# Optimization experiments

Measured on AMD Instinct MI355X. Metric: run time of the kernel, lower is better.

## Reference

```python
import jax, jax.numpy as jnp
import numpy as np

L, H, C = 2, 2, 128            # conv layers, heads, out_channels
N, E, B = 10000, 100000, 64    # nodes, edges, graphs
F_NODE, F_EDGE, FC = 92, 50, 512
HC, C3 = H * C, 3 * C


def _ln(x, g, b, eps=1e-5):
    m = x.mean(-1, keepdims=True)
    v = jnp.var(x, axis=-1, keepdims=True)
    return (x - m) * jax.lax.rsqrt(v + eps) * g + b


def setup_inputs() -> dict:
    key = jax.random.key(0)
    ks = jax.random.split(key, 20)
    r = lambda i, shape, s=0.05: jax.random.normal(ks[i], shape, jnp.float32) * s
    d = {}
    d["x"] = jax.random.normal(ks[0], (N, F_NODE), jnp.float32)
    d["edge_attr"] = jax.random.normal(ks[1], (E, F_EDGE), jnp.float32)
    d["pge"] = jax.random.normal(ks[2], (B, 32), jnp.float32)
    d["cse"] = jax.random.normal(ks[3], (B, 7), jnp.float32)
    d["edge_index"] = jax.random.randint(ks[4], (2, E), 0, N, jnp.int32)
    d["batch"] = jnp.sort(jax.random.randint(ks[5], (N,), 0, B, jnp.int32))
    d["atom_W"] = r(6, (F_NODE, C)); d["atom_b"] = jnp.zeros(C)
    d["edge_W"] = r(7, (F_EDGE, C)); d["edge_b"] = jnp.zeros(C)
    d["Wq"] = r(8, (L, C, HC)); d["bq"] = jnp.zeros((L, HC))
    d["Wk"] = r(9, (L, C, HC)); d["bk"] = jnp.zeros((L, HC))
    d["Wv"] = r(10, (L, C, HC)); d["bv"] = jnp.zeros((L, HC))
    d["We"] = r(11, (L, C, HC))
    d["Wmu"] = r(12, (L, C3, C3)); d["bmu"] = jnp.zeros((L, C3))
    d["Wm"] = r(13, (L, C3, C)); d["bm"] = jnp.zeros((L, C))
    d["ln_m_g"] = jnp.ones((L, C)); d["ln_m_b"] = jnp.zeros((L, C))
    d["ln_a_g"] = jnp.ones((L, C3)); d["ln_a_b"] = jnp.zeros((L, C3))
    d["Wc"] = r(14, (L, HC, C)); d["bc"] = jnp.zeros((L, C))
    d["bn_g"] = jnp.ones((L, C)); d["bn_b"] = jnp.zeros((L, C))
    d["Wskip"] = r(15, (L, C, C)); d["bskip"] = jnp.zeros((L, C))
    d["fc_W"] = r(16, (C + 32 + 7, FC)); d["fc_b"] = jnp.zeros(FC)
    d["out_W"] = r(17, (FC, 1)); d["out_b"] = jnp.zeros(1)
    return d


def reference(x, edge_attr, pge, cse, edge_index, batch, atom_W, atom_b,
              edge_W, edge_b, Wq, bq, Wk, bk, Wv, bv, We, Wmu, bmu, Wm, bm,
              ln_m_g, ln_m_b, ln_a_g, ln_a_b, Wc, bc, bn_g, bn_b, Wskip,
              bskip, fc_W, fc_b, out_W, out_b):
    src, dst = edge_index[0], edge_index[1]  # j = source, i = target
    nf = x @ atom_W + atom_b                 # [N, C]
    ef = edge_attr @ edge_W + edge_b         # [E, C]
    scale = 1.0 / np.sqrt(C3).astype(np.float32)
    for i in range(L):
        q = (nf @ Wq[i] + bq[i]).reshape(N, H, C)
        k = (nf @ Wk[i] + bk[i]).reshape(N, H, C)
        v = (nf @ Wv[i] + bv[i]).reshape(N, H, C)
        ea = (ef @ We[i]).reshape(E, H, C)
        qi = q[dst]
        qcat = jnp.concatenate([qi, qi, qi], -1)                 # [E,H,3C]
        kcat = jnp.concatenate([k[dst], k[src], ea], -1)         # [E,H,3C]
        alpha = qcat * kcat * scale
        gate = jax.nn.sigmoid(_ln(alpha, ln_a_g[i], ln_a_b[i]))
        m = jnp.concatenate([v[dst], v[src], ea], -1)            # [E,H,3C]
        m = (jnp.einsum('ehf,fg->ehg', m, Wmu[i]) + bmu[i]) * gate
        m = jnp.einsum('ehf,fc->ehc', m, Wm[i]) + bm[i]          # [E,H,C]
        m = _ln(m, ln_m_g[i], ln_m_b[i])
        agg = jax.ops.segment_sum(m, dst, num_segments=N)        # scatter-add
        o = agg.reshape(N, HC) @ Wc[i] + bc[i]                   # lin_concate
        mu = o.mean(0); var = jnp.var(o, axis=0)                 # BN (batch stats)
        o = (o - mu) * jax.lax.rsqrt(var + 1e-5) * bn_g[i] + bn_b[i]
        o = jax.nn.silu(o)
        nf = o + nf @ Wskip[i] + bskip[i]                        # root skip
    sums = jax.ops.segment_sum(nf, batch, num_segments=B)
    cnt = jax.ops.segment_sum(jnp.ones((N, 1), nf.dtype), batch, num_segments=B)
    pooled = sums / jnp.maximum(cnt, 1.0)                        # global_mean_pool
    feats = jnp.concatenate([pooled, pge, cse], 1)               # [B, C+39]
    h = jax.nn.silu(feats @ fc_W + fc_b)
    return h @ out_W + out_b                                     # [B, 1]
```

## Files before the change

### kernel.cpp

```cpp
#include <hip/hip_runtime.h>
#include <math.h>

#define N_NODES 10000
#define N_EDGES 100000
#define N_GRAPH 64
#define CDIM 128
#define HCDIM 256
#define C3DIM 384
#define QKPW 2176

typedef unsigned short u16;
typedef __attribute__((ext_vector_type(8))) short bf16x8;
typedef __attribute__((ext_vector_type(4))) float f32x4;

__device__ __forceinline__ u16 f2bf(float f) {
  union { float f; unsigned int u; } x; x.f = f;
  unsigned int u = x.u + 0x7fffu + ((x.u >> 16) & 1u);
  return (u16)(u >> 16);
}
__device__ __forceinline__ float bf2f(u16 h) {
  union { unsigned int u; float f; } x; x.u = ((unsigned int)h) << 16;
  return x.f;
}

template<int OUT_BF16, int DO_STATS, int A_F32>
__global__ __launch_bounds__(256) void mfma_gemm_kernel(
    const void* __restrict__ Ain, const u16* __restrict__ WT,
    const float* __restrict__ bias, void* __restrict__ Y,
    u16* __restrict__ Ymirror, float* __restrict__ cs, float* __restrict__ cs2,
    int M, int K, int N) {
  const int tid = threadIdx.x;
  const int w = tid >> 6, l = tid & 63;
  const int lq = l >> 4, ln = l & 15;
  const int bm = blockIdx.y * 128, bn = blockIdx.x * 64;
  int ra = bm + w * 32 + ln;      if (ra > M - 1) ra = M - 1;
  int rb = bm + w * 32 + 16 + ln; if (rb > M - 1) rb = M - 1;
  f32x4 acc[2][4];
#pragma unroll
  for (int g = 0; g < 2; ++g)
#pragma unroll
    for (int nt = 0; nt < 4; ++nt) acc[g][nt] = {0.f, 0.f, 0.f, 0.f};
  for (int k0 = 0; k0 < K; k0 += 32) {
    bf16x8 a0, a1;
    if (A_F32) {
      const float* Af = (const float*)Ain;
      f32x4 p0 = *(const f32x4*)&Af[(size_t)ra * K + k0 + lq * 8];
      f32x4 p1 = *(const f32x4*)&Af[(size_t)ra * K + k0 + lq * 8 + 4];
      f32x4 p2 = *(const f32x4*)&Af[(size_t)rb * K + k0 + lq * 8];
      f32x4 p3 = *(const f32x4*)&Af[(size_t)rb * K + k0 + lq * 8 + 4];
#pragma unroll
      for (int j = 0; j < 4; ++j) {
        a0[j] = (short)f2bf(p0[j]); a0[4 + j] = (short)f2bf(p1[j]);
        a1[j] = (short)f2bf(p2[j]); a1[4 + j] = (short)f2bf(p3[j]);
      }
    } else {
      const u16* Ab = (const u16*)Ain;
      a0 = *(const bf16x8*)&Ab[(size_t)ra * K + k0 + lq * 8];
      a1 = *(const bf16x8*)&Ab[(size_t)rb * K + k0 + lq * 8];
    }
#pragma unroll
    for (int nt = 0; nt < 4; ++nt) {
      bf16x8 b = *(const bf16x8*)&WT[(size_t)(bn + nt * 16 + ln) * K + k0 + lq * 8];
      acc[0][nt] = __builtin_amdgcn_mfma_f32_16x16x32_bf16(a0, b, acc[0][nt], 0, 0, 0);
      acc[1][nt] = __builtin_amdgcn_mfma_f32_16x16x32_bf16(a1, b, acc[1][nt], 0, 0, 0);
    }
  }
#pragma unroll
  for (int g = 0; g < 2; ++g) {
    int rowbase = bm + w * 32 + g * 16 + lq * 4;
#pragma unroll
    for (int nt = 0; nt < 4; ++nt) {
      int gn = bn + nt * 16 + ln;
      float bv = bias ? bias[gn] : 0.f;
#pragma unroll
      for (int r = 0; r < 4; ++r) {
        int gm = rowbase + r;
        if (gm < M) {
          float val = acc[g][nt][r] + bv;
          if (OUT_BF16) ((u16*)Y)[(size_t)gm * N + gn] = f2bf(val);
          else          ((float*)Y)[(size_t)gm * N + gn] = val;
          if (Ymirror)  Ymirror[(size_t)gm * N + gn] = f2bf(val);
        }
      }
    }
  }
  if (DO_STATS) {
#pragma unroll
    for (int nt = 0; nt < 4; ++nt) {
      int gn = bn + nt * 16 + ln;
      float bv = bias ? bias[gn] : 0.f;
      float s = 0.f, s2 = 0.f;
#pragma unroll
      for (int g = 0; g < 2; ++g) {
        int rowbase = bm + w * 32 + g * 16 + lq * 4;
#pragma unroll
        for (int r = 0; r < 4; ++r) {
          if (rowbase + r < M) {
            float v = acc[g][nt][r] + bv;
            s += v; s2 += v * v;
          }
        }
      }
      s += __shfl_xor(s, 16); s2 += __shfl_xor(s2, 16);
      s += __shfl_xor(s, 32); s2 += __shfl_xor(s2, 32);
      if (lq == 0) { atomicAdd(&cs[gn], s); atomicAdd(&cs2[gn], s2); }
    }
  }
}

__global__ void pack_init_kernel(
    const float* __restrict__ x, const float* __restrict__ ea,
    const float* __restrict__ atom_W, const float* __restrict__ edge_W,
    u16* __restrict__ xpad, u16* __restrict__ epad,
    u16* __restrict__ atomWT, u16* __restrict__ WeT2) {
  int z = blockIdx.y;
  int idx0 = blockIdx.x * 256 + threadIdx.x;
  const int stride = 256 * 256;
  if (z == 0) {
    for (int idx = idx0; idx < N_NODES * 96; idx += stride) {
      int n = idx / 96, k = idx - n * 96;
      xpad[idx] = (k < 92) ? f2bf(x[(size_t)n * 92 + k]) : (u16)0;
    }
  } else if (z == 1) {
    for (int idx = idx0; idx < N_EDGES * 64; idx += stride) {
      int e = idx >> 6, k = idx & 63;
      epad[idx] = (k < 50) ? f2bf(ea[(size_t)e * 50 + k]) : (u16)0;
    }
  } else if (z == 2) {
    if (idx0 < 128 * 96) { int n = idx0 / 96, k = idx0 - n * 96;
      atomWT[idx0] = (k < 92) ? f2bf(atom_W[(size_t)k * 128 + n]) : (u16)0; }
  } else {
    if (idx0 < 128 * 64) { int n = idx0 >> 6, k = idx0 & 63;
      WeT2[idx0] = (k < 50) ? f2bf(edge_W[(size_t)k * 128 + n]) : (u16)0; }
  }
}

__global__ __launch_bounds__(256) void prep_kernel(
    const float* __restrict__ Wv, const float* __restrict__ We_l,
    const float* __restrict__ Wmu,
    const float* __restrict__ Wq, const float* __restrict__ Wk,
    const float* __restrict__ Wc, const float* __restrict__ Wsk,
    const float* __restrict__ Wm_l, const float* __restrict__ bmu,
    const float* __restrict__ bv_l,
    const float* __restrict__ bq_l, const float* __restrict__ bk_l,
    const float* __restrict__ bsk_l,
    u16* __restrict__ WallT, u16* __restrict__ WcT, u16* __restrict__ WcTw,
    u16* __restrict__ WmTb, float* __restrict__ cbv, float* __restrict__ ball,
    float* __restrict__ agg, float* __restrict__ cs, float* __restrict__ cs2) {
  __shared__ float As[16][68];
  __shared__ float Bs[16][65];
  const int b = blockIdx.x;
  const int tid = threadIdx.x;
  if (b < 72) {
    const int zc = b / 12, rem = b % 12;
    const int by = rem / 6, bx = rem % 6;
    const float* Ap; const float* Bp; u16* Cp; int colbase;
    if (zc < 4) {
      int part = zc >> 1, h = zc & 1;
      Ap = Wv + h * 128; Bp = Wmu + part * 128 * 384;
      Cp = WallT; colbase = 512 + part * 768 + h * 384;
    } else {
      int h = zc - 4;
      Ap = We_l + h * 128; Bp = Wmu + 256 * 384;
      Cp = WcT; colbase = 256 + h * 384;
    }
    const int bm = by * 64, bn = bx * 64;
    const int tx = tid & 15, ty = tid >> 4;
    float acc[4][4] = {};
    for (int k0 = 0; k0 < 128; k0 += 16) {
#pragma unroll
      for (int i = 0; i < 4; ++i) {
        int l = tid + i * 256;
        int kk = l & 15, m = l >> 4;
        As[kk][m] = Ap[(size_t)(bm + m) * 256 + k0 + kk];
      }
#pragma unroll
      for (int i = 0; i < 4; ++i) {
        int l = tid + i * 256;
        int n = l & 63, kk = l >> 6;
        Bs[kk][n] = Bp[(size_t)(k0 + kk) * 384 + bn + n];
      }
      __syncthreads();
#pragma unroll
      for (int kk = 0; kk < 16; ++kk) {
        float a[4], bb[4];
#pragma unroll
        for (int i = 0; i < 4; ++i) a[i] = As[kk][ty * 4 + i];
#pragma unroll
        for (int j = 0; j < 4; ++j) bb[j] = Bs[kk][tx * 4 + j];
#pragma unroll
        for (int i = 0; i < 4; ++i)
#pragma unroll
          for (int j = 0; j < 4; ++j) acc[i][j] += a[i] * bb[j];
      }
      __syncthreads();
    }
#pragma unroll
    for (int i = 0; i < 4; ++i) {
      int gk = bm + ty * 4 + i;
#pragma unroll
      for (int j = 0; j < 4; ++j) {
        int gcol = colbase + bn + tx * 4 + j;
        Cp[(size_t)gcol * 128 + gk] = f2bf(acc[i][j]);
      }
    }
    return;
  }
  const int pb = b - 72;
  const int z = pb / 192;
  const int idx = (pb % 192) * 256 + tid;
  if (z == 0) {
    if (idx < 32768) { int col = idx >> 7, kk = idx & 127;
      WallT[(size_t)col * 128 + kk] = f2bf(Wq[(size_t)kk * 256 + col]); }
  } else if (z == 1) {
    if (idx < 32768) { int col = idx >> 7, kk = idx & 127;
      WallT[(size_t)(256 + col) * 128 + kk] = f2bf(Wk[(size_t)kk * 256 + col]); }
  } else if (z == 2) {
    if (idx < 32768) { int col = idx >> 8, kk = idx & 255;
      WcTw[(size_t)col * 256 + kk] = f2bf(Wc[(size_t)kk * 128 + col]); }
  } else if (z == 3) {
    if (idx < 16384) { int col = idx >> 7, kk = idx & 127;
      WallT[(size_t)(2048 + col) * 128 + kk] = f2bf(Wsk[(size_t)kk * 128 + col]); }
  } else if (z == 4) {
    if (idx < 49152) { int col = idx / 384, kk = idx - col * 384;
      WmTb[idx] = f2bf(Wm_l[(size_t)kk * 128 + col]); }
  } else if (z == 5) {
    if (idx < 768) {
      int h2 = idx / 384, g = idx - h2 * 384;
      float s = bmu[g];
      for (int d = 0; d < 128; ++d)
        s += bv_l[h2 * 128 + d] * (Wmu[(size_t)d * 384 + g] + Wmu[(size_t)(128 + d) * 384 + g]);
      cbv[idx] = s;
    }
  } else if (z == 6) {
    if (idx < QKPW) {
      float v = 0.f;
      if (idx < 256) v = bq_l[idx];
      else if (idx < 512) v = bk_l[idx - 256];
      else if (idx >= 2048) v = bsk_l[idx - 2048];
      ball[idx] = v;
    }
  } else if (z == 7) {
    for (int p = idx; p < N_NODES * HCDIM; p += 192 * 256) agg[p] = 0.f;
    if (idx < 128) { cs[idx] = 0.f; cs2[idx] = 0.f; }
  } else {
    if (idx < 32768) { int col = idx >> 7, kk = idx & 127;
      WcT[(size_t)col * 128 + kk] = f2bf(We_l[(size_t)kk * 256 + col]); }
  }
}

#define C1S 520
__global__ __launch_bounds__(256, 5) void edge_kernel(
    const u16* __restrict__ qkp, const u16* __restrict__ efb,
    const int* __restrict__ ei, const u16* __restrict__ WcT,
    const float* __restrict__ cbv,
    const float* __restrict__ lag, const float* __restrict__ lab,
    const u16* __restrict__ WmT, const float* __restrict__ bm_l,
    const float* __restrict__ lmg, const float* __restrict__ lmb,
    float* __restrict__ agg, int E) {
  __shared__ __align__(16) u16 C1[16 * C1S];
  __shared__ __align__(16) u16 A2p[12 * 512];
  __shared__ int did16[16];
  float* C2 = (float*)A2p;
  const int tid = threadIdx.x;
  const int h = blockIdx.x & 1;
  const int e0 = (blockIdx.x >> 1) * 16;
  const int w = tid >> 6, l = tid & 63;
  const int lq = l >> 4, ln = l & 15;
  const float scale = 0.051031036307982884f;

  if (tid < 16) did16[tid] = ei[E + e0 + tid];

  const int r = tid >> 4, lx = tid & 15;

  bf16x8 qv, kdv, ksv, pdv[3], psv[3];
  {
    int edge = e0 + r;
    int dstn = ei[E + edge], srcn = ei[edge];
    const u16* db = qkp + (size_t)dstn * QKPW;
    const u16* sb = qkp + (size_t)srcn * QKPW;
    qv  = *(const bf16x8*)&db[h * 128 + lx * 8];
    kdv = *(const bf16x8*)&db[256 + h * 128 + lx * 8];
    ksv = *(const bf16x8*)&sb[256 + h * 128 + lx * 8];
#pragma unroll
    for (int p = 0; p < 3; ++p) {
      pdv[p] = *(const bf16x8*)&db[512 + h * 384 + p * 128 + lx * 8];
      psv[p] = *(const bf16x8*)&sb[512 + 768 + h * 384 + p * 128 + lx * 8];
    }
  }

  {
    bf16x8 afr[4];
    const u16* ab = efb + (size_t)(e0 + ln) * 128 + lq * 8;
#pragma unroll
    for (int ks = 0; ks < 4; ++ks) afr[ks] = *(const bf16x8*)(ab + ks * 32);
#pragma unroll 2
    for (int nt = 0; nt < 8; ++nt) {
      int col0 = (w * 8 + nt) * 16;
      int wc = (col0 < 128) ? h * 128 + col0 : 256 + h * 384 + (col0 - 128);
      const u16* bb = WcT + (size_t)(wc + ln) * 128 + lq * 8;
      f32x4 acc = {0.f, 0.f, 0.f, 0.f};
#pragma unroll
      for (int ks = 0; ks < 4; ++ks)
        acc = __builtin_amdgcn_mfma_f32_16x16x32_bf16(
            afr[ks], *(const bf16x8*)(bb + ks * 32), acc, 0, 0, 0);
      int col = col0 + ln;
#pragma unroll
      for (int rr = 0; rr < 4; ++rr) C1[(lq * 4 + rr) * C1S + col] = f2bf(acc[rr]);
    }
  }
  __syncthreads();

  {
    bf16x8 sea = *(const bf16x8*)&C1[r * C1S + lx * 8];
    float a0[8], a1[8], a2[8];
    float sacc = 0.f, s2acc = 0.f;
#pragma unroll
    for (int j = 0; j < 8; ++j) {
      float qf = bf2f((u16)qv[j]);
      float x0 = qf * bf2f((u16)kdv[j]) * scale;
      float x1 = qf * bf2f((u16)ksv[j]) * scale;
      float x2 = qf * bf2f((u16)sea[j]) * scale;
      a0[j] = x0; a1[j] = x1; a2[j] = x2;
      sacc += x0 + x1 + x2;
      s2acc += x0 * x0 + x1 * x1 + x2 * x2;
    }
#pragma unroll
    for (int mm = 1; mm < 16; mm <<= 1) {
      sacc += __shfl_xor(sacc, mm); s2acc += __shfl_xor(s2acc, mm);
    }
    float mean = sacc * (1.f / C3DIM);
    float rstd = rsqrtf(s2acc * (1.f / C3DIM) - mean * mean + 1e-5f);
#pragma unroll
    for (int p = 0; p < 3; ++p) {
      const float* lg = lag + p * 128 + lx * 8;
      const float* lb = lab + p * 128 + lx * 8;
      f32x4 g0 = *(const f32x4*)lg, g1 = *(const f32x4*)(lg + 4);
      f32x4 b0 = *(const f32x4*)lb, b1 = *(const f32x4*)(lb + 4);
      f32x4 c0 = *(const f32x4*)&cbv[h * 384 + p * 128 + lx * 8];
      f32x4 c1 = *(const f32x4*)&cbv[h * 384 + p * 128 + lx * 8 + 4];
      bf16x8 pe = *(const bf16x8*)&C1[r * C1S + 128 + p * 128 + lx * 8];
      bf16x8 outv;
#pragma unroll
      for (int j = 0; j < 8; ++j) {
        float av = p == 0 ? a0[j] : (p == 1 ? a1[j] : a2[j]);
        float gg = j < 4 ? g0[j] : g1[j - 4];
        float bb2 = j < 4 ? b0[j] : b1[j - 4];
        float cbj = j < 4 ? c0[j] : c1[j - 4];
        float z = (av - mean) * rstd * gg + bb2;
        float gate = 1.f / (1.f + expf(-z));
        float t = (bf2f((u16)pe[j]) + bf2f((u16)pdv[p][j]) +
                   bf2f((u16)psv[p][j]) + cbj) * gate;
        outv[j] = (short)f2bf(t);
      }
      int ks = p * 4 + (lx >> 2), qq = lx & 3;
      int slot = (((r ^ (qq << 2)) + ks) & 15) | (qq << 4);
      *(bf16x8*)&A2p[ks * 512 + slot * 8] = outv;
    }
  }
  __syncthreads();

  {
    bf16x8 af2[12];
#pragma unroll
    for (int ks = 0; ks < 12; ++ks) {
      int slot = (((ln ^ (lq << 2)) + ks) & 15) | (lq << 4);
      af2[ks] = *(const bf16x8*)&A2p[ks * 512 + slot * 8];
    }
    __syncthreads();
#pragma unroll
    for (int nt = 0; nt < 2; ++nt) {
      int g = w * 2 + nt;
      const u16* bb = WmT + (size_t)(g * 16 + ln) * 384 + lq * 8;
      f32x4 acc = {0.f, 0.f, 0.f, 0.f};
#pragma unroll
      for (int ks = 0; ks < 12; ++ks)
        acc = __builtin_amdgcn_mfma_f32_16x16x32_bf16(
            af2[ks], *(const bf16x8*)(bb + ks * 32), acc, 0, 0, 0);
      int col = g * 16 + ln;
      float bcol = bm_l[col];
#pragma unroll
      for (int rr = 0; rr < 4; ++rr) C2[(lq * 4 + rr) * 132 + col] = acc[rr] + bcol;
    }
  }
  __syncthreads();

  {
    for (int rw = w; rw < 16; rw += 4) {
      float v0 = C2[rw * 132 + l], v1 = C2[rw * 132 + l + 64];
      float sa = v0 + v1, s2a = v0 * v0 + v1 * v1;
#pragma unroll
      for (int off2 = 32; off2 > 0; off2 >>= 1) {
        sa += __shfl_down(sa, off2); s2a += __shfl_down(s2a, off2);
      }
      sa = __shfl(sa, 0); s2a = __shfl(s2a, 0);
      float mean = sa * (1.f / CDIM);
      float rstd = rsqrtf(s2a * (1.f / CDIM) - mean * mean + 1e-5f);
      int dstn = did16[rw];
      float o0 = (v0 - mean) * rstd * lmg[l] + lmb[l];
      float o1 = (v1 - mean) * rstd * lmg[l + 64] + lmb[l + 64];
      atomicAdd(&agg[(size_t)dstn * HCDIM + h * CDIM + l], o0);
      atomicAdd(&agg[(size_t)dstn * HCDIM + h * CDIM + l + 64], o1);
    }
  }
}

__global__ void bn_silu_skip_kernel(
    const float* __restrict__ o, const u16* __restrict__ qkp,
    const float* __restrict__ cs, const float* __restrict__ cs2,
    const float* __restrict__ g, const float* __restrict__ b,
    float* __restrict__ nf, u16* __restrict__ nfb) {
  int idx = blockIdx.x * blockDim.x + threadIdx.x;
  if (idx >= N_NODES * CDIM) return;
  int c = idx & (CDIM - 1);
  int n = idx >> 7;
  float m = cs[c] * (1.f / N_NODES);
  float var = cs2[c] * (1.f / N_NODES) - m * m;
  float rstd = rsqrtf(var + 1e-5f);
  float x = (o[idx] - m) * rstd * g[c] + b[c];
  float sig = 1.f / (1.f + expf(-x));
  float skipv = bf2f(qkp[(size_t)n * QKPW + 2048 + c]);
  float val = x * sig + skipv;
  nf[idx] = val;
  nfb[idx] = f2bf(val);
}

__global__ __launch_bounds__(256) void poolfeats_kernel(
    const float* __restrict__ nf, const int* __restrict__ batch,
    const float* __restrict__ pge, const float* __restrict__ cse,
    float* __restrict__ feats) {
  const int b = blockIdx.x, tid = threadIdx.x;
  int lo = 0, hi = N_NODES;
  {
    int L = 0, R = N_NODES;
    while (L < R) { int m2 = (L + R) >> 1; if (batch[m2] < b) L = m2 + 1; else R = m2; }
    lo = L;
    L = lo; R = N_NODES;
    while (L < R) { int m2 = (L + R) >> 1; if (batch[m2] <= b) L = m2 + 1; else R = m2; }
    hi = L;
  }
  __shared__ float sacc[2][128];
  const int half = tid >> 7, c = tid & 127;
  float s = 0.f;
  for (int n = lo + half; n < hi; n += 2) s += nf[(size_t)n * CDIM + c];
  sacc[half][c] = s;
  __syncthreads();
  float cntf = fmaxf((float)(hi - lo), 1.f);
  if (tid < 128) feats[b * 167 + tid] = (sacc[0][tid] + sacc[1][tid]) / cntf;
  else if (tid < 160) feats[b * 167 + 128 + (tid - 128)] = pge[b * 32 + (tid - 128)];
  else if (tid < 167) feats[b * 167 + 160 + (tid - 160)] = cse[b * 7 + (tid - 160)];
}

__global__ __launch_bounds__(256) void fcout_kernel(
    const float* __restrict__ feats, const float* __restrict__ fc_W,
    const float* __restrict__ fc_b, const float* __restrict__ ow,
    const float* __restrict__ ob, float* __restrict__ out) {
  const int b = blockIdx.x, tid = threadIdx.x;
  __shared__ float sf[167];
  if (tid < 167) sf[tid] = feats[b * 167 + tid];
  __syncthreads();
  float acc0 = fc_b[tid], acc1 = fc_b[tid + 256];
  for (int k = 0; k < 167; ++k) {
    float fv = sf[k];
    acc0 += fv * fc_W[(size_t)k * 512 + tid];
    acc1 += fv * fc_W[(size_t)k * 512 + tid + 256];
  }
  float h0 = acc0 / (1.f + expf(-acc0));
  float h1 = acc1 / (1.f + expf(-acc1));
  float s = h0 * ow[tid] + h1 * ow[tid + 256];
  __shared__ float red[4];
#pragma unroll
  for (int off = 32; off > 0; off >>= 1) s += __shfl_down(s, off);
  if ((tid & 63) == 0) red[tid >> 6] = s;
  __syncthreads();
  if (tid == 0) out[b] = red[0] + red[1] + red[2] + red[3] + ob[0];
}

extern "C" void kernel_launch(void* const* d_in, const int* in_sizes, int n_in,
                              void* d_out, int out_size, void* d_ws, size_t ws_size,
                              hipStream_t stream) {
  const float* x         = (const float*)d_in[0];
  const float* edge_attr = (const float*)d_in[1];
  const float* pge       = (const float*)d_in[2];
  const float* cse       = (const float*)d_in[3];
  const int*   ei        = (const int*)d_in[4];
  const int*   batch     = (const int*)d_in[5];
  const float* atom_W    = (const float*)d_in[6];
  const float* atom_b    = (const float*)d_in[7];
  const float* edge_W    = (const float*)d_in[8];
  const float* edge_b    = (const float*)d_in[9];
  const float* Wq        = (const float*)d_in[10];
  const float* bq        = (const float*)d_in[11];
  const float* Wk        = (const float*)d_in[12];
  const float* bk        = (const float*)d_in[13];
  const float* Wv        = (const float*)d_in[14];
  const float* bv        = (const float*)d_in[15];
  const float* We        = (const float*)d_in[16];
  const float* Wmu       = (const float*)d_in[17];
  const float* bmu       = (const float*)d_in[18];
  const float* Wm        = (const float*)d_in[19];
  const float* bm        = (const float*)d_in[20];
  const float* ln_m_g    = (const float*)d_in[21];
  const float* ln_m_b    = (const float*)d_in[22];
  const float* ln_a_g    = (const float*)d_in[23];
  const float* ln_a_b    = (const float*)d_in[24];
  const float* Wc        = (const float*)d_in[25];
  const float* bc        = (const float*)d_in[26];
  const float* bn_g      = (const float*)d_in[27];
  const float* bn_b      = (const float*)d_in[28];
  const float* Wskip     = (const float*)d_in[29];
  const float* bskip     = (const float*)d_in[30];
  const float* fc_W      = (const float*)d_in[31];
  const float* fc_b      = (const float*)d_in[32];
  const float* out_W     = (const float*)d_in[33];
  const float* out_b     = (const float*)d_in[34];

  float* ws = (float*)d_ws;
  size_t off = 0;
  float* nf    = ws + off; off += (size_t)N_NODES * CDIM;
  float* agg   = ws + off; off += (size_t)N_NODES * HCDIM;
  float* o     = ws + off; off += (size_t)N_NODES * CDIM;
  float* cbv   = ws + off; off += 768;
  float* ball  = ws + off; off += QKPW;
  float* csum  = ws + off; off += CDIM;
  float* csum2 = ws + off; off += CDIM;
  float* feats = ws + off; off += (size_t)N_GRAPH * 167;
  u16* efb   = (u16*)(ws + off); off += (size_t)N_EDGES * 64;
  u16* WcT   = (u16*)(ws + off); off += 65536;
  u16* WmTb  = (u16*)(ws + off); off += 24576;
  u16* nfb   = (u16*)(ws + off); off += (size_t)N_NODES * 64;
  u16* qkp   = (u16*)(ws + off); off += (size_t)N_NODES * (QKPW/2);
  u16* WallT = (u16*)(ws + off); off += (size_t)QKPW * 64;
  u16* WcTw  = (u16*)(ws + off); off += 16384;
  u16* xpad  = (u16*)(ws + off); off += (size_t)N_NODES * 48;
  u16* epad  = (u16*)(ws + off); off += (size_t)N_EDGES * 32;
  u16* atomWT= (u16*)(ws + off); off += 6144;
  u16* WeT2  = (u16*)(ws + off); off += 4096;

  pack_init_kernel<<<dim3(256, 4), 256, 0, stream>>>(x, edge_attr, atom_W, edge_W,
                                                     xpad, epad, atomWT, WeT2);
  mfma_gemm_kernel<0, 0, 0><<<dim3(2, 79), 256, 0, stream>>>(
      xpad, atomWT, atom_b, nf, nfb, nullptr, nullptr, N_NODES, 96, CDIM);
  mfma_gemm_kernel<1, 0, 0><<<dim3(2, 782), 256, 0, stream>>>(
      epad, WeT2, edge_b, efb, nullptr, nullptr, nullptr, N_EDGES, 64, CDIM);

  for (int i = 0; i < 2; ++i) {
    prep_kernel<<<dim3(1800), 256, 0, stream>>>(
        Wv + (size_t)i * CDIM * HCDIM, We + (size_t)i * CDIM * HCDIM,
        Wmu + (size_t)i * C3DIM * C3DIM,
        Wq + (size_t)i * CDIM * HCDIM, Wk + (size_t)i * CDIM * HCDIM,
        Wc + (size_t)i * HCDIM * CDIM, Wskip + (size_t)i * CDIM * CDIM,
        Wm + (size_t)i * C3DIM * CDIM, bmu + i * C3DIM, bv + i * HCDIM,
        bq + i * HCDIM, bk + i * HCDIM, bskip + i * CDIM,
        WallT, WcT, WcTw, WmTb, cbv, ball, agg, csum, csum2);

    mfma_gemm_kernel<1, 0, 0><<<dim3(QKPW / 64, 79), 256, 0, stream>>>(
        nfb, WallT, ball, qkp, nullptr, nullptr, nullptr, N_NODES, CDIM, QKPW);

    edge_kernel<<<dim3(N_EDGES / 16 * 2), dim3(256), 0, stream>>>(
        qkp, efb, ei, WcT, cbv,
        ln_a_g + i * C3DIM, ln_a_b + i * C3DIM,
        WmTb, bm + i * CDIM,
        ln_m_g + i * CDIM, ln_m_b + i * CDIM, agg, N_EDGES);

    mfma_gemm_kernel<0, 1, 1><<<dim3(2, 79), 256, 0, stream>>>(
        agg, WcTw, bc + i * CDIM, o, nullptr, csum, csum2, N_NODES, HCDIM, CDIM);

    bn_silu_skip_kernel<<<dim3((N_NODES * CDIM + 255) / 256), dim3(256), 0, stream>>>(
        o, qkp, csum, csum2, bn_g + i * CDIM, bn_b + i * CDIM, nf, nfb);
  }

  poolfeats_kernel<<<dim3(N_GRAPH), 256, 0, stream>>>(nf, batch, pge, cse, feats);
  fcout_kernel<<<dim3(N_GRAPH), 256, 0, stream>>>(feats, fc_W, fc_b, out_W, out_b,
                                                  (float*)d_out);
}
```

Baseline: 1.171 ms.

## Make edge kernel persistent over edge groups with prefetch of next gathers

The edge kernel now loops each block over ten consecutive (edge-group, head) tiles instead of one. The next tile's indices are loaded early, and its q/k/projection rows are gathered while the current tile's second GEMM and LayerNorm run, so the gather latency overlaps compute. LayerNorm constants are hoisted out of the loop, occupancy is reduced to 4 blocks per SIMD, and expf is replaced by __expf in several kernels. The trade-off is fewer blocks, higher register pressure, and a small accuracy change from the faster exp.

```diff
diff --git a/kernel.cpp b/kernel.cpp
--- a/kernel.cpp
+++ b/kernel.cpp
@@ -250,7 +250,8 @@
 }
 
 #define C1S 520
-__global__ __launch_bounds__(256, 5) void edge_kernel(
+#define NITER 10
+__global__ __launch_bounds__(256, 4) void edge_kernel(
     const u16* __restrict__ qkp, const u16* __restrict__ efb,
     const int* __restrict__ ei, const u16* __restrict__ WcT,
     const float* __restrict__ cbv,
@@ -260,23 +261,21 @@
     float* __restrict__ agg, int E) {
   __shared__ __align__(16) u16 C1[16 * C1S];
   __shared__ __align__(16) u16 A2p[12 * 512];
-  __shared__ int did16[16];
   float* C2 = (float*)A2p;
   const int tid = threadIdx.x;
-  const int h = blockIdx.x & 1;
-  const int e0 = (blockIdx.x >> 1) * 16;
   const int w = tid >> 6, l = tid & 63;
   const int lq = l >> 4, ln = l & 15;
+  const int r = tid >> 4, lx = tid & 15;
   const float scale = 0.051031036307982884f;
-
-  if (tid < 16) did16[tid] = ei[E + e0 + tid];
-
-  const int r = tid >> 4, lx = tid & 15;
+  const int gbase = blockIdx.x * NITER;
+  const float lg0 = lmg[l], lg1 = lmg[l + 64];
+  const float lb0 = lmb[l], lb1 = lmb[l + 64];
 
   bf16x8 qv, kdv, ksv, pdv[3], psv[3];
   {
-    int edge = e0 + r;
-    int dstn = ei[E + edge], srcn = ei[edge];
+    const int group = gbase;
+    const int h = group & 1, e0 = (group >> 1) * 16;
+    int dstn = ei[E + e0 + r], srcn = ei[e0 + r];
     const u16* db = qkp + (size_t)dstn * QKPW;
     const u16* sb = qkp + (size_t)srcn * QKPW;
     qv  = *(const bf16x8*)&db[h * 128 + lx * 8];
@@ -289,118 +288,147 @@
     }
   }
 
-  {
-    bf16x8 afr[4];
-    const u16* ab = efb + (size_t)(e0 + ln) * 128 + lq * 8;
-#pragma unroll
-    for (int ks = 0; ks < 4; ++ks) afr[ks] = *(const bf16x8*)(ab + ks * 32);
+  for (int it = 0; it < NITER; ++it) {
+    const int group = gbase + it;
+    const int h = group & 1;
+    const int e0 = (group >> 1) * 16;
+
+    int ndst = 0, nsrc = 0;
+    if (it + 1 < NITER) {
+      int ne0 = ((group + 1) >> 1) * 16;
+      ndst = ei[E + ne0 + r];
+      nsrc = ei[ne0 + r];
+    }
+
+    {
+      bf16x8 afr[4];
+      const u16* ab = efb + (size_t)(e0 + ln) * 128 + lq * 8;
+#pragma unroll
+      for (int ks = 0; ks < 4; ++ks) afr[ks] = *(const bf16x8*)(ab + ks * 32);
 #pragma unroll 2
-    for (int nt = 0; nt < 8; ++nt) {
-      int col0 = (w * 8 + nt) * 16;
-      int wc = (col0 < 128) ? h * 128 + col0 : 256 + h * 384 + (col0 - 128);
-      const u16* bb = WcT + (size_t)(wc + ln) * 128 + lq * 8;
-      f32x4 acc = {0.f, 0.f, 0.f, 0.f};
-#pragma unroll
-      for (int ks = 0; ks < 4; ++ks)
-        acc = __builtin_amdgcn_mfma_f32_16x16x32_bf16(
-            afr[ks], *(const bf16x8*)(bb + ks * 32), acc, 0, 0, 0);
-      int col = col0 + ln;
-#pragma unroll
-      for (int rr = 0; rr < 4; ++rr) C1[(lq * 4 + rr) * C1S + col] = f2bf(acc[rr]);
-    }
-  }
-  __syncthreads();
-
-  {
-    bf16x8 sea = *(const bf16x8*)&C1[r * C1S + lx * 8];
-    float a0[8], a1[8], a2[8];
-    float sacc = 0.f, s2acc = 0.f;
-#pragma unroll
-    for (int j = 0; j < 8; ++j) {
-      float qf = bf2f((u16)qv[j]);
-      float x0 = qf * bf2f((u16)kdv[j]) * scale;
-      float x1 = qf * bf2f((u16)ksv[j]) * scale;
-      float x2 = qf * bf2f((u16)sea[j]) * scale;
-      a0[j] = x0; a1[j] = x1; a2[j] = x2;
-      sacc += x0 + x1 + x2;
-      s2acc += x0 * x0 + x1 * x1 + x2 * x2;
-    }
-#pragma unroll
-    for (int mm = 1; mm < 16; mm <<= 1) {
-      sacc += __shfl_xor(sacc, mm); s2acc += __shfl_xor(s2acc, mm);
-    }
-    float mean = sacc * (1.f / C3DIM);
-    float rstd = rsqrtf(s2acc * (1.f / C3DIM) - mean * mean + 1e-5f);
-#pragma unroll
-    for (int p = 0; p < 3; ++p) {
-      const float* lg = lag + p * 128 + lx * 8;
-      const float* lb = lab + p * 128 + lx * 8;
-      f32x4 g0 = *(const f32x4*)lg, g1 = *(const f32x4*)(lg + 4);
-      f32x4 b0 = *(const f32x4*)lb, b1 = *(const f32x4*)(lb + 4);
-      f32x4 c0 = *(const f32x4*)&cbv[h * 384 + p * 128 + lx * 8];
-      f32x4 c1 = *(const f32x4*)&cbv[h * 384 + p * 128 + lx * 8 + 4];
-      bf16x8 pe = *(const bf16x8*)&C1[r * C1S + 128 + p * 128 + lx * 8];
-      bf16x8 outv;
+      for (int nt = 0; nt < 8; ++nt) {
+        int col0 = (w * 8 + nt) * 16;
+        int wc = (col0 < 128) ? h * 128 + col0 : 256 + h * 384 + (col0 - 128);
+        const u16* bb = WcT + (size_t)(wc + ln) * 128 + lq * 8;
+        f32x4 acc = {0.f, 0.f, 0.f, 0.f};
+#pragma unroll
+        for (int ks = 0; ks < 4; ++ks)
+          acc = __builtin_amdgcn_mfma_f32_16x16x32_bf16(
+              afr[ks], *(const bf16x8*)(bb + ks * 32), acc, 0, 0, 0);
+        int col = col0 + ln;
+#pragma unroll
+        for (int rr = 0; rr < 4; ++rr) C1[(lq * 4 + rr) * C1S + col] = f2bf(acc[rr]);
+      }
+    }
+    __syncthreads();
+
+    {
+      bf16x8 sea = *(const bf16x8*)&C1[r * C1S + lx * 8];
+      float a0[8], a1[8], a2[8];
+      float sacc = 0.f, s2acc = 0.f;
 #pragma unroll
       for (int j = 0; j < 8; ++j) {
-        float av = p == 0 ? a0[j] : (p == 1 ? a1[j] : a2[j]);
-        float gg = j < 4 ? g0[j] : g1[j - 4];
-        float bb2 = j < 4 ? b0[j] : b1[j - 4];
-        float cbj = j < 4 ? c0[j] : c1[j - 4];
-        float z = (av - mean) * rstd * gg + bb2;
-        float gate = 1.f / (1.f + expf(-z));
-        float t = (bf2f((u16)pe[j]) + bf2f((u16)pdv[p][j]) +
-                   bf2f((u16)psv[p][j]) + cbj) * gate;
-        outv[j] = (short)f2bf(t);
-      }
-      int ks = p * 4 + (lx >> 2), qq = lx & 3;
-      int slot = (((r ^ (qq << 2)) + ks) & 15) | (qq << 4);
-      *(bf16x8*)&A2p[ks * 512 + slot * 8] = outv;
-    }
-  }
-  __syncthreads();
-
-  {
-    bf16x8 af2[12];
-#pragma unroll
-    for (int ks = 0; ks < 12; ++ks) {
-      int slot = (((ln ^ (lq << 2)) + ks) & 15) | (lq << 4);
-      af2[ks] = *(const bf16x8*)&A2p[ks * 512 + slot * 8];
+        float qf = bf2f((u16)qv[j]);
+        float x0 = qf * bf2f((u16)kdv[j]) * scale;
+        float x1 = qf * bf2f((u16)ksv[j]) * scale;
+        float x2 = qf * bf2f((u16)sea[j]) * scale;
+        a0[j] = x0; a1[j] = x1; a2[j] = x2;
+        sacc += x0 + x1 + x2;
+        s2acc += x0 * x0 + x1 * x1 + x2 * x2;
+      }
+#pragma unroll
+      for (int mm = 1; mm < 16; mm <<= 1) {
+        sacc += __shfl_xor(sacc, mm); s2acc += __shfl_xor(s2acc, mm);
+      }
+      float mean = sacc * (1.f / C3DIM);
+      float rstd = rsqrtf(s2acc * (1.f / C3DIM) - mean * mean + 1e-5f);
+#pragma unroll
+      for (int p = 0; p < 3; ++p) {
+        const float* lg = lag + p * 128 + lx * 8;
+        const float* lb = lab + p * 128 + lx * 8;
+        f32x4 g0 = *(const f32x4*)lg, g1 = *(const f32x4*)(lg + 4);
+        f32x4 b0 = *(const f32x4*)lb, b1 = *(const f32x4*)(lb + 4);
+        f32x4 c0 = *(const f32x4*)&cbv[h * 384 + p * 128 + lx * 8];
+        f32x4 c1 = *(const f32x4*)&cbv[h * 384 + p * 128 + lx * 8 + 4];
+        bf16x8 pe = *(const bf16x8*)&C1[r * C1S + 128 + p * 128 + lx * 8];
+        bf16x8 outv;
+#pragma unroll
+        for (int j = 0; j < 8; ++j) {
+          float av = p == 0 ? a0[j] : (p == 1 ? a1[j] : a2[j]);
+          float gg = j < 4 ? g0[j] : g1[j - 4];
+          float bb2 = j < 4 ? b0[j] : b1[j - 4];
+          float cbj = j < 4 ? c0[j] : c1[j - 4];
+          float z = (av - mean) * rstd * gg + bb2;
+          float gate = 1.f / (1.f + __expf(-z));
+          float t = (bf2f((u16)pe[j]) + bf2f((u16)pdv[p][j]) +
+                     bf2f((u16)psv[p][j]) + cbj) * gate;
+          outv[j] = (short)f2bf(t);
+        }
+        int ks = p * 4 + (lx >> 2), qq = lx & 3;
+        int slot = (((r ^ (qq << 2)) + ks) & 15) | (qq << 4);
+        *(bf16x8*)&A2p[ks * 512 + slot * 8] = outv;
+      }
+    }
+
+    if (it + 1 < NITER) {
+      const int nh = (group + 1) & 1;
+      const u16* db = qkp + (size_t)ndst * QKPW;
+      const u16* sb = qkp + (size_t)nsrc * QKPW;
+      qv  = *(const bf16x8*)&db[nh * 128 + lx * 8];
+      kdv = *(const bf16x8*)&db[256 + nh * 128 + lx * 8];
+      ksv = *(const bf16x8*)&sb[256 + nh * 128 + lx * 8];
+#pragma unroll
+      for (int p = 0; p < 3; ++p) {
+        pdv[p] = *(const bf16x8*)&db[512 + nh * 384 + p * 128 + lx * 8];
+        psv[p] = *(const bf16x8*)&sb[512 + 768 + nh * 384 + p * 128 + lx * 8];
+      }
     }
     __syncthreads();
-#pragma unroll
-    for (int nt = 0; nt < 2; ++nt) {
-      int g = w * 2 + nt;
-      const u16* bb = WmT + (size_t)(g * 16 + ln) * 384 + lq * 8;
-      f32x4 acc = {0.f, 0.f, 0.f, 0.f};
-#pragma unroll
-      for (int ks = 0; ks < 12; ++ks)
-        acc = __builtin_amdgcn_mfma_f32_16x16x32_bf16(
-            af2[ks], *(const bf16x8*)(bb + ks * 32), acc, 0, 0, 0);
-      int col = g * 16 + ln;
-      float bcol = bm_l[col];
-#pragma unroll
-      for (int rr = 0; rr < 4; ++rr) C2[(lq * 4 + rr) * 132 + col] = acc[rr] + bcol;
-    }
-  }
-  __syncthreads();
-
-  {
-    for (int rw = w; rw < 16; rw += 4) {
-      float v0 = C2[rw * 132 + l], v1 = C2[rw * 132 + l + 64];
-      float sa = v0 + v1, s2a = v0 * v0 + v1 * v1;
-#pragma unroll
-      for (int off2 = 32; off2 > 0; off2 >>= 1) {
-        sa += __shfl_down(sa, off2); s2a += __shfl_down(s2a, off2);
-      }
-      sa = __shfl(sa, 0); s2a = __shfl(s2a, 0);
-      float mean = sa * (1.f / CDIM);
-      float rstd = rsqrtf(s2a * (1.f / CDIM) - mean * mean + 1e-5f);
-      int dstn = did16[rw];
-      float o0 = (v0 - mean) * rstd * lmg[l] + lmb[l];
-      float o1 = (v1 - mean) * rstd * lmg[l + 64] + lmb[l + 64];
-      atomicAdd(&agg[(size_t)dstn * HCDIM + h * CDIM + l], o0);
-      atomicAdd(&agg[(size_t)dstn * HCDIM + h * CDIM + l + 64], o1);
+
+    {
+      bf16x8 af2[12];
+#pragma unroll
+      for (int ks = 0; ks < 12; ++ks) {
+        int slot = (((ln ^ (lq << 2)) + ks) & 15) | (lq << 4);
+        af2[ks] = *(const bf16x8*)&A2p[ks * 512 + slot * 8];
+      }
+      __syncthreads();
+#pragma unroll
+      for (int nt = 0; nt < 2; ++nt) {
+        int g = w * 2 + nt;
+        const u16* bb = WmT + (size_t)(g * 16 + ln) * 384 + lq * 8;
+        f32x4 acc = {0.f, 0.f, 0.f, 0.f};
+#pragma unroll
+        for (int ks = 0; ks < 12; ++ks)
+          acc = __builtin_amdgcn_mfma_f32_16x16x32_bf16(
+              af2[ks], *(const bf16x8*)(bb + ks * 32), acc, 0, 0, 0);
+        int col = g * 16 + ln;
+        float bcol = bm_l[col];
+#pragma unroll
+        for (int rr = 0; rr < 4; ++rr) C2[(lq * 4 + rr) * 132 + col] = acc[rr] + bcol;
+      }
+    }
+    __syncthreads();
+
+    {
+#pragma unroll
+      for (int i4 = 0; i4 < 4; ++i4) {
+        int rw = w * 4 + i4;
+        float v0 = C2[rw * 132 + l], v1 = C2[rw * 132 + l + 64];
+        float sa = v0 + v1, s2a = v0 * v0 + v1 * v1;
+#pragma unroll
+        for (int off2 = 32; off2 > 0; off2 >>= 1) {
+          sa += __shfl_down(sa, off2); s2a += __shfl_down(s2a, off2);
+        }
+        sa = __shfl(sa, 0); s2a = __shfl(s2a, 0);
+        float mean = sa * (1.f / CDIM);
+        float rstd = rsqrtf(s2a * (1.f / CDIM) - mean * mean + 1e-5f);
+        int dstn = ei[E + e0 + rw];
+        float o0 = (v0 - mean) * rstd * lg0 + lb0;
+        float o1 = (v1 - mean) * rstd * lg1 + lb1;
+        atomicAdd(&agg[(size_t)dstn * HCDIM + h * CDIM + l], o0);
+        atomicAdd(&agg[(size_t)dstn * HCDIM + h * CDIM + l + 64], o1);
+      }
     }
   }
 }
@@ -418,7 +446,7 @@
   float var = cs2[c] * (1.f / N_NODES) - m * m;
   float rstd = rsqrtf(var + 1e-5f);
   float x = (o[idx] - m) * rstd * g[c] + b[c];
-  float sig = 1.f / (1.f + expf(-x));
+  float sig = 1.f / (1.f + __expf(-x));
   float skipv = bf2f(qkp[(size_t)n * QKPW + 2048 + c]);
   float val = x * sig + skipv;
   nf[idx] = val;
@@ -465,8 +493,8 @@
     acc0 += fv * fc_W[(size_t)k * 512 + tid];
     acc1 += fv * fc_W[(size_t)k * 512 + tid + 256];
   }
-  float h0 = acc0 / (1.f + expf(-acc0));
-  float h1 = acc1 / (1.f + expf(-acc1));
+  float h0 = acc0 / (1.f + __expf(-acc0));
+  float h1 = acc1 / (1.f + __expf(-acc1));
   float s = h0 * ow[tid] + h1 * ow[tid + 256];
   __shared__ float red[4];
 #pragma unroll
@@ -557,7 +585,7 @@
     mfma_gemm_kernel<1, 0, 0><<<dim3(QKPW / 64, 79), 256, 0, stream>>>(
         nfb, WallT, ball, qkp, nullptr, nullptr, nullptr, N_NODES, CDIM, QKPW);
 
-    edge_kernel<<<dim3(N_EDGES / 16 * 2), dim3(256), 0, stream>>>(
+    edge_kernel<<<dim3(N_EDGES / 16 * 2 / NITER), dim3(256), 0, stream>>>(
         qkp, efb, ei, WcT, cbv,
         ln_a_g + i * C3DIM, ln_a_b + i * C3DIM,
         WmTb, bm + i * CDIM,
```

New measurement: 1.935 ms. 65.2% more time.
